# Kernel optimization log

Measured on AMD Instinct MI355X. Metric: run time of the kernel, lower is better.

Reference implementation:

```python
import jax, jax.numpy as jnp
import numpy as np


def setup_inputs() -> dict:
    key = jax.random.key(0)
    k1, k2, k3, k4 = jax.random.split(key, 4)
    N, C_in, C_out, H, W, K = 32, 128, 256, 56, 56, 3
    x = jax.random.normal(k1, (N, C_in, H, W), dtype=jnp.float32)
    # ternary weights in {-1, 0, +1}, stored as int8 like the torch buffer
    w_q = jax.random.randint(k2, (C_out, C_in, K, K), -1, 2).astype(jnp.int8)
    s = jax.random.uniform(k3, (C_out, 1, 1), dtype=jnp.float32) + 0.5
    bias = jax.random.normal(k4, (C_out,), dtype=jnp.float32)
    return {"x": x, "w_q": w_q, "s": s, "bias": bias}


def reference(x, w_q, s, bias):
    # y = conv2d(x, w_q.float()) * s + bias, stride=1, padding=1, dilation=1, groups=1
    w = w_q.astype(x.dtype)  # ternary {-1,0,+1} cast to float, as in torch
    y = jax.lax.conv_general_dilated(
        x, w,
        window_strides=(1, 1),
        padding=((1, 1), (1, 1)),
        lhs_dilation=(1, 1),
        rhs_dilation=(1, 1),
        dimension_numbers=("NCHW", "OIHW", "NCHW"),
        feature_group_count=1,
    )
    y = y * s  # s: [C_out,1,1] broadcasts over [N,C_out,H,W]
    y = y + bias.reshape(1, -1, 1, 1)
    return y
```

## Files before the change

### kernel.cpp

```cpp
#include <hip/hip_runtime.h>
#include <hip/hip_bf16.h>

typedef unsigned short ushort_t;

#define N_IMG 32
#define C_IN  128
#define C_OUT 256
#define H_SZ  56
#define W_SZ  56
#define HW_SZ (H_SZ * W_SZ)
#define K_TOT (C_IN * 9)
#define WP 64
#define HP 58
#define ROW_E (WP * C_IN)

typedef __attribute__((ext_vector_type(8))) short bf16x8;
typedef __attribute__((ext_vector_type(4))) float floatx4;

__device__ __forceinline__ void gl_lds16(const ushort_t* g, ushort_t* l) {
  __builtin_amdgcn_global_load_lds(
      (const __attribute__((address_space(1))) void*)g,
      (__attribute__((address_space(3))) void*)l, 16, 0, 0);
}

__device__ __forceinline__ ushort_t f2bf(float f) {
  __hip_bfloat16 b = __float2bfloat16(f);
  return *reinterpret_cast<ushort_t*>(&b);
}

__global__ void wtrans_kernel(const int* __restrict__ wq, ushort_t* __restrict__ wt) {
  int idx = blockIdx.x * 256 + threadIdx.x;
  if (idx >= C_OUT * K_TOT) return;
  int co = idx / K_TOT;
  int k  = idx - co * K_TOT;
  int tap = k >> 7;
  int c   = k & 127;
  int kh = tap / 3, kw = tap - kh * 3;
  int v = wq[((co * C_IN + c) * 3 + kh) * 3 + kw];
  wt[idx] = f2bf((float)v);
}

__global__ __launch_bounds__(256) void xpad_kernel(const float* __restrict__ x,
                                                   ushort_t* __restrict__ xp) {
  int b = blockIdx.x;
  int t = threadIdx.x;
  ushort_t* row = xp + (size_t)b * ROW_E;
  int n = b / HP;
  int h1 = b - n * HP;
  if (b >= N_IMG * HP || h1 == 0 || h1 == HP - 1) {
    uint4 z = {0u, 0u, 0u, 0u};
    uint4* r4 = (uint4*)row;
#pragma unroll
    for (int i = 0; i < 4; ++i) r4[i * 256 + t] = z;
    return;
  }
  __shared__ float tile[C_IN * 57];
  int h = h1 - 1;
  const float* xb = x + (size_t)n * C_IN * HW_SZ + h * W_SZ;
#pragma unroll
  for (int i = 0; i < 7; ++i) {
    int idx = i * 256 + t;
    int c = idx / 14, f = idx - c * 14;
    float4 v = *(const float4*)(xb + (size_t)c * HW_SZ + f * 4);
    float* dst = &tile[c * 57 + f * 4];
    dst[0] = v.x; dst[1] = v.y; dst[2] = v.z; dst[3] = v.w;
  }
  __syncthreads();
  unsigned int* r32 = (unsigned int*)row;
#pragma unroll
  for (int i = 0; i < 16; ++i) {
    int idx = i * 256 + t;
    int wp = idx >> 6, cp = idx & 63;
    unsigned int u = 0;
    if (wp >= 1 && wp <= W_SZ) {
      int w = wp - 1;
      u = (unsigned int)f2bf(tile[(2 * cp) * 57 + w]) |
          ((unsigned int)f2bf(tile[(2 * cp + 1) * 57 + w]) << 16);
    }
    r32[wp * 64 + cp] = u;
  }
}

__global__ __launch_bounds__(256) void bitconv_kernel(
    const ushort_t* __restrict__ wt, const ushort_t* __restrict__ xp,
    const float* __restrict__ s, const float* __restrict__ bias,
    float* __restrict__ out) {
  __shared__ ushort_t As[2][128 * 64];
  __shared__ ushort_t Bs[2][128 * 64];

  int d = blockIdx.x;
  int xcd = d & 7;
  int r   = d >> 3;
  int co0 = (r & 1) * 128;
  int sp_tile = xcd * 112 + (r >> 1);
  int nh0 = sp_tile * 2;
  int n  = nh0 / H_SZ;
  int hh = nh0 - n * H_SZ;

  int tid  = threadIdx.x;
  int lane = tid & 63;
  int wid  = tid >> 6;
  int l15  = lane & 15;
  int quad = lane >> 4;
  int wave_m = (wid >> 1) * 64;
  int wave_n = (wid & 1) * 64;

  int qoff = (((lane & 7) ^ (lane >> 3)) * 8);
  const ushort_t* a_src[4];
  const ushort_t* b_src[4];
  int dst_e[4];
#pragma unroll
  for (int g = 0; g < 4; ++g) {
    int rrow = wid * 32 + g * 8 + (lane >> 3);
    a_src[g] = wt + (size_t)(co0 + rrow) * K_TOT + qoff;
    int hrow = rrow >> 6, wpp = (rrow & 63) + 1;
    b_src[g] = xp + (size_t)((n * HP + hh + 1 + hrow) * WP + wpp) * C_IN + qoff;
    dst_e[g] = (wid * 32 + g * 8) * 64;
  }

  int koff0 = (quad ^ (l15 & 7)) * 8;
  int koff1 = koff0 ^ 32;

  floatx4 acc[4][4];
#pragma unroll
  for (int mi = 0; mi < 4; ++mi)
#pragma unroll
    for (int ni = 0; ni < 4; ++ni)
      acc[mi][ni] = (floatx4){0.f, 0.f, 0.f, 0.f};

  auto stage = [&](int tap, int half, int buf) {
    int aoff = tap * C_IN + half * 64;
    int boff = (tap / 3 - 1) * ROW_E + (tap % 3 - 1) * C_IN + half * 64;
#pragma unroll
    for (int g = 0; g < 4; ++g) {
      gl_lds16(a_src[g] + aoff, &As[buf][dst_e[g]]);
      gl_lds16(b_src[g] + boff, &Bs[buf][dst_e[g]]);
    }
  };

  stage(0, 0, 0);
#pragma unroll
  for (int st = 0; st < 18; ++st) {
    int buf = st & 1;
    if (st < 17) {
      stage((st + 1) >> 1, (st + 1) & 1, buf ^ 1);
      asm volatile("s_waitcnt vmcnt(8)" ::: "memory");
    } else {
      asm volatile("s_waitcnt vmcnt(0)" ::: "memory");
    }
    __builtin_amdgcn_s_barrier();
    asm volatile("" ::: "memory");

#pragma unroll
    for (int ks = 0; ks < 2; ++ks) {
      int ko = ks ? koff1 : koff0;
      bf16x8 af[4], bfv[4];
#pragma unroll
      for (int mi = 0; mi < 4; ++mi)
        af[mi] = *(const bf16x8*)&As[buf][(wave_m + mi * 16 + l15) * 64 + ko];
#pragma unroll
      for (int ni = 0; ni < 4; ++ni)
        bfv[ni] = *(const bf16x8*)&Bs[buf][(wave_n + ni * 16 + l15) * 64 + ko];
#pragma unroll
      for (int mi = 0; mi < 4; ++mi)
#pragma unroll
        for (int ni = 0; ni < 4; ++ni)
          acc[mi][ni] = __builtin_amdgcn_mfma_f32_16x16x32_bf16(
              af[mi], bfv[ni], acc[mi][ni], 0, 0, 0);
    }

    asm volatile("" ::: "memory");
    __builtin_amdgcn_s_barrier();
    asm volatile("" ::: "memory");
  }

  int h_out = hh + (wid & 1);
#pragma unroll
  for (int mi = 0; mi < 4; ++mi) {
#pragma unroll
    for (int rg = 0; rg < 4; ++rg) {
      int co = co0 + wave_m + mi * 16 + quad * 4 + rg;
      float sv = s[co];
      float bv = bias[co];
      float* ob = out + (size_t)(n * C_OUT + co) * HW_SZ + h_out * W_SZ;
#pragma unroll
      for (int ni = 0; ni < 4; ++ni) {
        int wpp = ni * 16 + l15;
        if (wpp < W_SZ)
          ob[wpp] = acc[mi][ni][rg] * sv + bv;
      }
    }
  }
}

extern "C" void kernel_launch(void* const* d_in, const int* in_sizes, int n_in,
                              void* d_out, int out_size, void* d_ws, size_t ws_size,
                              hipStream_t stream) {
  const float* x    = (const float*)d_in[0];
  const int*   wq   = (const int*)d_in[1];
  const float* s    = (const float*)d_in[2];
  const float* bias = (const float*)d_in[3];
  float* out = (float*)d_out;

  char* ws = (char*)d_ws;
  ushort_t* wt = (ushort_t*)ws;
  ushort_t* xp = (ushort_t*)(ws + 589824);

  hipLaunchKernelGGL(wtrans_kernel, dim3((C_OUT * K_TOT) / 256), dim3(256), 0, stream,
                     wq, wt);
  hipLaunchKernelGGL(xpad_kernel, dim3(N_IMG * HP + 1), dim3(256), 0, stream, x, xp);
  hipLaunchKernelGGL(bitconv_kernel, dim3(1792), dim3(256), 0, stream,
                     wt, xp, s, bias, out);
}
```

Measured before the change: 216.7 us.

## Enlarge conv GEMM tile to 256x256 with 8-wave ping-pong MFMA schedule

Moves the bitconv kernel from 128x128 tiles with 4 waves to 256x256 tiles (all output channels by four image rows) with 8 waves per 512-thread block. The main loop becomes a ping-pong schedule that interleaves LDS fragment loads, staged global-to-LDS copies, barriers and setprio-raised MFMA bursts across four quadrant sub-steps. The aim is more data reuse per loaded byte and better overlap of memory traffic with matrix math. In exchange it uses 128 KB of LDS, more accumulator registers and only 448 blocks, which may leave CUs underused.

```diff
diff --git a/kernel.cpp b/kernel.cpp
--- a/kernel.cpp
+++ b/kernel.cpp
@@ -81,113 +81,202 @@
   }
 }
 
-__global__ __launch_bounds__(256) void bitconv_kernel(
+__global__ __launch_bounds__(512, 2) void bitconv_kernel(
     const ushort_t* __restrict__ wt, const ushort_t* __restrict__ xp,
     const float* __restrict__ s, const float* __restrict__ bias,
     float* __restrict__ out) {
-  __shared__ ushort_t As[2][128 * 64];
-  __shared__ ushort_t Bs[2][128 * 64];
+  __shared__ ushort_t As[2 * 16384];
+  __shared__ ushort_t Bs[2 * 16384];
 
   int d = blockIdx.x;
-  int xcd = d & 7;
-  int r   = d >> 3;
-  int co0 = (r & 1) * 128;
-  int sp_tile = xcd * 112 + (r >> 1);
-  int nh0 = sp_tile * 2;
-  int n  = nh0 / H_SZ;
-  int hh = nh0 - n * H_SZ;
+  int sp_tile = (d & 7) * 56 + (d >> 3);
 
   int tid  = threadIdx.x;
   int lane = tid & 63;
   int wid  = tid >> 6;
   int l15  = lane & 15;
   int quad = lane >> 4;
-  int wave_m = (wid >> 1) * 64;
-  int wave_n = (wid & 1) * 64;
-
-  int qoff = (((lane & 7) ^ (lane >> 3)) * 8);
-  const ushort_t* a_src[4];
-  const ushort_t* b_src[4];
-  int dst_e[4];
-#pragma unroll
-  for (int g = 0; g < 4; ++g) {
-    int rrow = wid * 32 + g * 8 + (lane >> 3);
-    a_src[g] = wt + (size_t)(co0 + rrow) * K_TOT + qoff;
-    int hrow = rrow >> 6, wpp = (rrow & 63) + 1;
-    b_src[g] = xp + (size_t)((n * HP + hh + 1 + hrow) * WP + wpp) * C_IN + qoff;
-    dst_e[g] = (wid * 32 + g * 8) * 64;
-  }
-
-  int koff0 = (quad ^ (l15 & 7)) * 8;
-  int koff1 = koff0 ^ 32;
-
-  floatx4 acc[4][4];
-#pragma unroll
-  for (int mi = 0; mi < 4; ++mi)
+  int wave_m = (wid >> 2) * 128;
+  int wave_n = (wid & 3) * 64;
+
+  int qoff = ((lane & 7) ^ (lane >> 3)) * 8;
+  const ushort_t* a_base = wt + (size_t)(tid >> 3) * K_TOT + qoff;
+  const ushort_t* b_base[2][2];
+#pragma unroll
+  for (int h = 0; h < 2; ++h)
+#pragma unroll
+    for (int s2 = 0; s2 < 2; ++s2) {
+      int nh = sp_tile * 4 + h * 2 + s2;
+      int n  = nh / H_SZ, hi = nh - n * H_SZ;
+      b_base[h][s2] =
+          xp + (size_t)((n * HP + 1 + hi) * WP + (tid >> 3) + 1) * C_IN + qoff;
+    }
+  int sd00 = (0 * 128 + 0 * 64 + wid * 8) * 64;
+  int sd01 = (0 * 128 + 1 * 64 + wid * 8) * 64;
+  int sd10 = (1 * 128 + 0 * 64 + wid * 8) * 64;
+  int sd11 = (1 * 128 + 1 * 64 + wid * 8) * 64;
+
+  int ko0 = (quad ^ (l15 & 7)) * 8;
+  int ko1 = ko0 ^ 32;
+  int ar = (wave_m + l15) * 64;
+  int br = (wave_n + l15) * 64;
+
+  floatx4 acc[8][4];
+#pragma unroll
+  for (int mi = 0; mi < 8; ++mi)
 #pragma unroll
     for (int ni = 0; ni < 4; ++ni)
       acc[mi][ni] = (floatx4){0.f, 0.f, 0.f, 0.f};
 
-  auto stage = [&](int tap, int half, int buf) {
-    int aoff = tap * C_IN + half * 64;
-    int boff = (tap / 3 - 1) * ROW_E + (tap % 3 - 1) * C_IN + half * 64;
-#pragma unroll
-    for (int g = 0; g < 4; ++g) {
-      gl_lds16(a_src[g] + aoff, &As[buf][dst_e[g]]);
-      gl_lds16(b_src[g] + boff, &Bs[buf][dst_e[g]]);
-    }
+  auto stageA = [&](int NB, int s_aoff) {
+    gl_lds16(a_base + 0 * K_TOT + s_aoff,                 &As[NB + sd00]);
+    gl_lds16(a_base + 64 * K_TOT + s_aoff,                &As[NB + sd01]);
+    gl_lds16(a_base + 128 * K_TOT + s_aoff,               &As[NB + sd10]);
+    gl_lds16(a_base + 192 * K_TOT + s_aoff,               &As[NB + sd11]);
   };
-
-  stage(0, 0, 0);
-#pragma unroll
-  for (int st = 0; st < 18; ++st) {
-    int buf = st & 1;
-    if (st < 17) {
-      stage((st + 1) >> 1, (st + 1) & 1, buf ^ 1);
-      asm volatile("s_waitcnt vmcnt(8)" ::: "memory");
+  auto stageB = [&](int NB, int s_boff) {
+    gl_lds16(b_base[0][0] + s_boff, &Bs[NB + sd00]);
+    gl_lds16(b_base[0][1] + s_boff, &Bs[NB + sd01]);
+    gl_lds16(b_base[1][0] + s_boff, &Bs[NB + sd10]);
+    gl_lds16(b_base[1][1] + s_boff, &Bs[NB + sd11]);
+  };
+
+  auto tile = [&](int AB, int NB, int s_aoff, int s_boff, bool do_stage) {
+    bf16x8 af[4][2], bn0[2][2], bn1[2][2];
+    if (do_stage) {
+      stageA(NB, s_aoff);
+      asm volatile("s_waitcnt vmcnt(4)" ::: "memory");
     } else {
       asm volatile("s_waitcnt vmcnt(0)" ::: "memory");
     }
     __builtin_amdgcn_s_barrier();
     asm volatile("" ::: "memory");
-
-#pragma unroll
-    for (int ks = 0; ks < 2; ++ks) {
-      int ko = ks ? koff1 : koff0;
-      bf16x8 af[4], bfv[4];
-#pragma unroll
-      for (int mi = 0; mi < 4; ++mi)
-        af[mi] = *(const bf16x8*)&As[buf][(wave_m + mi * 16 + l15) * 64 + ko];
-#pragma unroll
-      for (int ni = 0; ni < 4; ++ni)
-        bfv[ni] = *(const bf16x8*)&Bs[buf][(wave_n + ni * 16 + l15) * 64 + ko];
-#pragma unroll
-      for (int mi = 0; mi < 4; ++mi)
-#pragma unroll
-        for (int ni = 0; ni < 4; ++ni)
+#pragma unroll
+    for (int mi = 0; mi < 4; ++mi) {
+      af[mi][0] = *(const bf16x8*)&As[AB + ar + mi * 1024 + ko0];
+      af[mi][1] = *(const bf16x8*)&As[AB + ar + mi * 1024 + ko1];
+    }
+#pragma unroll
+    for (int ni = 0; ni < 2; ++ni) {
+      bn0[ni][0] = *(const bf16x8*)&Bs[AB + br + ni * 1024 + ko0];
+      bn0[ni][1] = *(const bf16x8*)&Bs[AB + br + ni * 1024 + ko1];
+    }
+    asm volatile("s_waitcnt lgkmcnt(0)" ::: "memory");
+    __builtin_amdgcn_sched_barrier(0);
+    __builtin_amdgcn_s_setprio(1);
+#pragma unroll
+    for (int mi = 0; mi < 4; ++mi)
+#pragma unroll
+      for (int ni = 0; ni < 2; ++ni)
+#pragma unroll
+        for (int ks = 0; ks < 2; ++ks)
           acc[mi][ni] = __builtin_amdgcn_mfma_f32_16x16x32_bf16(
-              af[mi], bfv[ni], acc[mi][ni], 0, 0, 0);
-    }
-
-    asm volatile("" ::: "memory");
-    __builtin_amdgcn_s_barrier();
-    asm volatile("" ::: "memory");
-  }
-
-  int h_out = hh + (wid & 1);
-#pragma unroll
-  for (int mi = 0; mi < 4; ++mi) {
+              af[mi][ks], bn0[ni][ks], acc[mi][ni], 0, 0, 0);
+    __builtin_amdgcn_s_setprio(0);
+    asm volatile("" ::: "memory");
+    __builtin_amdgcn_s_barrier();
+    asm volatile("" ::: "memory");
+#pragma unroll
+    for (int ni = 0; ni < 2; ++ni) {
+      bn1[ni][0] = *(const bf16x8*)&Bs[AB + br + (2 + ni) * 1024 + ko0];
+      bn1[ni][1] = *(const bf16x8*)&Bs[AB + br + (2 + ni) * 1024 + ko1];
+    }
+    if (do_stage) stageB(NB, s_boff);
+    asm volatile("" ::: "memory");
+    __builtin_amdgcn_s_barrier();
+    asm volatile("s_waitcnt lgkmcnt(0)" ::: "memory");
+    __builtin_amdgcn_sched_barrier(0);
+    __builtin_amdgcn_s_setprio(1);
+#pragma unroll
+    for (int mi = 0; mi < 4; ++mi)
+#pragma unroll
+      for (int ni = 0; ni < 2; ++ni)
+#pragma unroll
+        for (int ks = 0; ks < 2; ++ks)
+          acc[mi][2 + ni] = __builtin_amdgcn_mfma_f32_16x16x32_bf16(
+              af[mi][ks], bn1[ni][ks], acc[mi][2 + ni], 0, 0, 0);
+    __builtin_amdgcn_s_setprio(0);
+    asm volatile("" ::: "memory");
+    __builtin_amdgcn_s_barrier();
+    asm volatile("" ::: "memory");
+#pragma unroll
+    for (int mi = 0; mi < 4; ++mi) {
+      af[mi][0] = *(const bf16x8*)&As[AB + ar + (4 + mi) * 1024 + ko0];
+      af[mi][1] = *(const bf16x8*)&As[AB + ar + (4 + mi) * 1024 + ko1];
+    }
+    asm volatile("" ::: "memory");
+    __builtin_amdgcn_s_barrier();
+    asm volatile("s_waitcnt lgkmcnt(0)" ::: "memory");
+    __builtin_amdgcn_sched_barrier(0);
+    __builtin_amdgcn_s_setprio(1);
+#pragma unroll
+    for (int mi = 0; mi < 4; ++mi)
+#pragma unroll
+      for (int ni = 0; ni < 2; ++ni)
+#pragma unroll
+        for (int ks = 0; ks < 2; ++ks)
+          acc[4 + mi][2 + ni] = __builtin_amdgcn_mfma_f32_16x16x32_bf16(
+              af[mi][ks], bn1[ni][ks], acc[4 + mi][2 + ni], 0, 0, 0);
+    __builtin_amdgcn_s_setprio(0);
+    asm volatile("" ::: "memory");
+    __builtin_amdgcn_s_barrier();
+    asm volatile("" ::: "memory");
+#pragma unroll
+    for (int ni = 0; ni < 2; ++ni) {
+      bn0[ni][0] = *(const bf16x8*)&Bs[AB + br + ni * 1024 + ko0];
+      bn0[ni][1] = *(const bf16x8*)&Bs[AB + br + ni * 1024 + ko1];
+    }
+    asm volatile("" ::: "memory");
+    __builtin_amdgcn_s_barrier();
+    asm volatile("s_waitcnt lgkmcnt(0)" ::: "memory");
+    __builtin_amdgcn_sched_barrier(0);
+    __builtin_amdgcn_s_setprio(1);
+#pragma unroll
+    for (int mi = 0; mi < 4; ++mi)
+#pragma unroll
+      for (int ni = 0; ni < 2; ++ni)
+#pragma unroll
+        for (int ks = 0; ks < 2; ++ks)
+          acc[4 + mi][ni] = __builtin_amdgcn_mfma_f32_16x16x32_bf16(
+              af[mi][ks], bn0[ni][ks], acc[4 + mi][ni], 0, 0, 0);
+    __builtin_amdgcn_s_setprio(0);
+    asm volatile("" ::: "memory");
+    __builtin_amdgcn_s_barrier();
+    asm volatile("" ::: "memory");
+  };
+
+  stageA(0, 0);
+  stageB(0, -ROW_E - C_IN);
+
+#pragma unroll 1
+  for (int kh = -1; kh <= 1; ++kh) {
+#pragma unroll 1
+    for (int kw = -1; kw <= 1; ++kw) {
+      int tapidx = (kh + 1) * 3 + (kw + 1);
+      bool last = (kh == 1) && (kw == 1);
+      int nkh = (kw == 1) ? kh + 1 : kh;
+      int nkw = (kw == 1) ? -1 : kw + 1;
+      tile(0, 16384, tapidx * 128 + 64, kh * ROW_E + kw * C_IN + 64, true);
+      tile(16384, 0, (tapidx + 1) * 128, nkh * ROW_E + nkw * C_IN, !last);
+    }
+  }
+
+  int nh_w = sp_tile * 4 + (wid & 3);
+  int n_out = nh_w / H_SZ, h_img = nh_w - n_out * H_SZ;
+  float* obase = out + (size_t)n_out * C_OUT * HW_SZ + h_img * W_SZ;
+#pragma unroll
+  for (int mi = 0; mi < 8; ++mi) {
 #pragma unroll
     for (int rg = 0; rg < 4; ++rg) {
-      int co = co0 + wave_m + mi * 16 + quad * 4 + rg;
+      int co = wave_m + mi * 16 + quad * 4 + rg;
       float sv = s[co];
       float bv = bias[co];
-      float* ob = out + (size_t)(n * C_OUT + co) * HW_SZ + h_out * W_SZ;
+      float* ob = obase + (size_t)co * HW_SZ;
 #pragma unroll
       for (int ni = 0; ni < 4; ++ni) {
-        int wpp = ni * 16 + l15;
-        if (wpp < W_SZ)
-          ob[wpp] = acc[mi][ni][rg] * sv + bv;
+        int w2 = ni * 16 + l15;
+        if (w2 < W_SZ)
+          ob[w2] = acc[mi][ni][rg] * sv + bv;
       }
     }
   }
@@ -209,6 +298,6 @@
   hipLaunchKernelGGL(wtrans_kernel, dim3((C_OUT * K_TOT) / 256), dim3(256), 0, stream,
                      wq, wt);
   hipLaunchKernelGGL(xpad_kernel, dim3(N_IMG * HP + 1), dim3(256), 0, stream, x, xp);
-  hipLaunchKernelGGL(bitconv_kernel, dim3(1792), dim3(256), 0, stream,
+  hipLaunchKernelGGL(bitconv_kernel, dim3(448), dim3(512), 0, stream,
                      wt, xp, s, bias, out);
 }
```

New measurement: 227.6 us. 5.0% more time.

## Enlarge conv GEMM tile to 256x256 with 512-thread blocks

Applied to the files above, without the earlier changes.

Each block now covers all 256 output channels and four spatial rows (256 pixels) using 8 waves, instead of a 128x128 tile with 4 waves. Each wave computes a 128x64 sub-tile with 8x4 accumulators, and the A fragment loads are split into two halves. The goal is to double operand reuse per LDS byte and cut redundant global loads of weights and activations. The cost is more registers per thread and more LDS (128KB double-buffered), and the grid shrinks to 448 blocks, which may underfill 256 CUs and limit occupancy.

```diff
diff --git a/kernel.cpp b/kernel.cpp
--- a/kernel.cpp
+++ b/kernel.cpp
@@ -81,69 +81,78 @@
   }
 }
 
-__global__ __launch_bounds__(256) void bitconv_kernel(
+__global__ __launch_bounds__(512, 2) void bitconv_kernel(
     const ushort_t* __restrict__ wt, const ushort_t* __restrict__ xp,
     const float* __restrict__ s, const float* __restrict__ bias,
     float* __restrict__ out) {
-  __shared__ ushort_t As[2][128 * 64];
-  __shared__ ushort_t Bs[2][128 * 64];
+  __shared__ ushort_t As[2 * 16384];
+  __shared__ ushort_t Bs[2 * 16384];
 
   int d = blockIdx.x;
-  int xcd = d & 7;
-  int r   = d >> 3;
-  int co0 = (r & 1) * 128;
-  int sp_tile = xcd * 112 + (r >> 1);
-  int nh0 = sp_tile * 2;
-  int n  = nh0 / H_SZ;
-  int hh = nh0 - n * H_SZ;
+  int sp_tile = (d & 7) * 56 + (d >> 3);
 
   int tid  = threadIdx.x;
   int lane = tid & 63;
   int wid  = tid >> 6;
   int l15  = lane & 15;
   int quad = lane >> 4;
-  int wave_m = (wid >> 1) * 64;
-  int wave_n = (wid & 1) * 64;
-
-  int qoff = (((lane & 7) ^ (lane >> 3)) * 8);
-  const ushort_t* a_src[4];
-  const ushort_t* b_src[4];
-  int dst_e[4];
-#pragma unroll
-  for (int g = 0; g < 4; ++g) {
-    int rrow = wid * 32 + g * 8 + (lane >> 3);
-    a_src[g] = wt + (size_t)(co0 + rrow) * K_TOT + qoff;
-    int hrow = rrow >> 6, wpp = (rrow & 63) + 1;
-    b_src[g] = xp + (size_t)((n * HP + hh + 1 + hrow) * WP + wpp) * C_IN + qoff;
-    dst_e[g] = (wid * 32 + g * 8) * 64;
-  }
-
-  int koff0 = (quad ^ (l15 & 7)) * 8;
-  int koff1 = koff0 ^ 32;
-
-  floatx4 acc[4][4];
-#pragma unroll
-  for (int mi = 0; mi < 4; ++mi)
+  int wave_m = (wid >> 2) * 128;
+  int wave_n = (wid & 3) * 64;
+
+  int qoff = ((lane & 7) ^ (lane >> 3)) * 8;
+  const ushort_t* a_base = wt + (size_t)(tid >> 3) * K_TOT + qoff;
+  const ushort_t* b_base[2][2];
+#pragma unroll
+  for (int h = 0; h < 2; ++h)
+#pragma unroll
+    for (int s2 = 0; s2 < 2; ++s2) {
+      int nh = sp_tile * 4 + h * 2 + s2;
+      int n  = nh / H_SZ, hi = nh - n * H_SZ;
+      b_base[h][s2] =
+          xp + (size_t)((n * HP + 1 + hi) * WP + (tid >> 3) + 1) * C_IN + qoff;
+    }
+  int sd0 = (0 * 64 + wid * 8) * 64;
+  int sd1 = (1 * 64 + wid * 8) * 64;
+  int sd2 = (2 * 64 + wid * 8) * 64;
+  int sd3 = (3 * 64 + wid * 8) * 64;
+
+  int ko0 = (quad ^ (l15 & 7)) * 8;
+  int ko1 = ko0 ^ 32;
+  int ar = (wave_m + l15) * 64;
+  int br = (wave_n + l15) * 64;
+
+  floatx4 acc[8][4];
+#pragma unroll
+  for (int mi = 0; mi < 8; ++mi)
 #pragma unroll
     for (int ni = 0; ni < 4; ++ni)
       acc[mi][ni] = (floatx4){0.f, 0.f, 0.f, 0.f};
 
-  auto stage = [&](int tap, int half, int buf) {
-    int aoff = tap * C_IN + half * 64;
-    int boff = (tap / 3 - 1) * ROW_E + (tap % 3 - 1) * C_IN + half * 64;
-#pragma unroll
-    for (int g = 0; g < 4; ++g) {
-      gl_lds16(a_src[g] + aoff, &As[buf][dst_e[g]]);
-      gl_lds16(b_src[g] + boff, &Bs[buf][dst_e[g]]);
-    }
+  auto stageA = [&](int NB, int s_aoff) {
+    gl_lds16(a_base + 0 * K_TOT + s_aoff,   &As[NB + sd0]);
+    gl_lds16(a_base + 64 * K_TOT + s_aoff,  &As[NB + sd1]);
+    gl_lds16(a_base + 128 * K_TOT + s_aoff, &As[NB + sd2]);
+    gl_lds16(a_base + 192 * K_TOT + s_aoff, &As[NB + sd3]);
   };
-
-  stage(0, 0, 0);
-#pragma unroll
-  for (int st = 0; st < 18; ++st) {
-    int buf = st & 1;
-    if (st < 17) {
-      stage((st + 1) >> 1, (st + 1) & 1, buf ^ 1);
+  auto stageB = [&](int NB, int s_boff) {
+    gl_lds16(b_base[0][0] + s_boff, &Bs[NB + sd0]);
+    gl_lds16(b_base[0][1] + s_boff, &Bs[NB + sd1]);
+    gl_lds16(b_base[1][0] + s_boff, &Bs[NB + sd2]);
+    gl_lds16(b_base[1][1] + s_boff, &Bs[NB + sd3]);
+  };
+
+  stageA(0, 0);
+  stageB(0, -ROW_E - C_IN);
+
+#pragma unroll
+  for (int kt = 0; kt < 18; ++kt) {
+    int cb = (kt & 1) * 16384;
+    int nb = 16384 - cb;
+    if (kt < 17) {
+      int ntap  = (kt + 1) >> 1;
+      int nhalf = (kt + 1) & 1;
+      stageA(nb, ntap * C_IN + nhalf * 64);
+      stageB(nb, (ntap / 3 - 1) * ROW_E + (ntap % 3 - 1) * C_IN + nhalf * 64);
       asm volatile("s_waitcnt vmcnt(8)" ::: "memory");
     } else {
       asm volatile("s_waitcnt vmcnt(0)" ::: "memory");
@@ -151,43 +160,60 @@
     __builtin_amdgcn_s_barrier();
     asm volatile("" ::: "memory");
 
-#pragma unroll
-    for (int ks = 0; ks < 2; ++ks) {
-      int ko = ks ? koff1 : koff0;
-      bf16x8 af[4], bfv[4];
-#pragma unroll
-      for (int mi = 0; mi < 4; ++mi)
-        af[mi] = *(const bf16x8*)&As[buf][(wave_m + mi * 16 + l15) * 64 + ko];
+    bf16x8 bfv[4][2], af[4][2];
+#pragma unroll
+    for (int ni = 0; ni < 4; ++ni) {
+      bfv[ni][0] = *(const bf16x8*)&Bs[cb + br + ni * 1024 + ko0];
+      bfv[ni][1] = *(const bf16x8*)&Bs[cb + br + ni * 1024 + ko1];
+    }
+#pragma unroll
+    for (int mi = 0; mi < 4; ++mi) {
+      af[mi][0] = *(const bf16x8*)&As[cb + ar + mi * 1024 + ko0];
+      af[mi][1] = *(const bf16x8*)&As[cb + ar + mi * 1024 + ko1];
+    }
+#pragma unroll
+    for (int mi = 0; mi < 4; ++mi)
 #pragma unroll
       for (int ni = 0; ni < 4; ++ni)
-        bfv[ni] = *(const bf16x8*)&Bs[buf][(wave_n + ni * 16 + l15) * 64 + ko];
-#pragma unroll
-      for (int mi = 0; mi < 4; ++mi)
-#pragma unroll
-        for (int ni = 0; ni < 4; ++ni)
+#pragma unroll
+        for (int ks = 0; ks < 2; ++ks)
           acc[mi][ni] = __builtin_amdgcn_mfma_f32_16x16x32_bf16(
-              af[mi], bfv[ni], acc[mi][ni], 0, 0, 0);
-    }
+              af[mi][ks], bfv[ni][ks], acc[mi][ni], 0, 0, 0);
+#pragma unroll
+    for (int mi = 0; mi < 4; ++mi) {
+      af[mi][0] = *(const bf16x8*)&As[cb + ar + (4 + mi) * 1024 + ko0];
+      af[mi][1] = *(const bf16x8*)&As[cb + ar + (4 + mi) * 1024 + ko1];
+    }
+#pragma unroll
+    for (int mi = 0; mi < 4; ++mi)
+#pragma unroll
+      for (int ni = 0; ni < 4; ++ni)
+#pragma unroll
+        for (int ks = 0; ks < 2; ++ks)
+          acc[4 + mi][ni] = __builtin_amdgcn_mfma_f32_16x16x32_bf16(
+              af[mi][ks], bfv[ni][ks], acc[4 + mi][ni], 0, 0, 0);
 
     asm volatile("" ::: "memory");
     __builtin_amdgcn_s_barrier();
     asm volatile("" ::: "memory");
   }
 
-  int h_out = hh + (wid & 1);
-#pragma unroll
-  for (int mi = 0; mi < 4; ++mi) {
+  int nh_w = sp_tile * 4 + (wid & 3);
+  int n_out = nh_w / H_SZ, h_img = nh_w - n_out * H_SZ;
+  float* obase = out + (size_t)n_out * C_OUT * HW_SZ + h_img * W_SZ;
+#pragma unroll
+  for (int mi = 0; mi < 8; ++mi) {
 #pragma unroll
     for (int rg = 0; rg < 4; ++rg) {
-      int co = co0 + wave_m + mi * 16 + quad * 4 + rg;
+      int co = wave_m + mi * 16 + quad * 4 + rg;
       float sv = s[co];
       float bv = bias[co];
-      float* ob = out + (size_t)(n * C_OUT + co) * HW_SZ + h_out * W_SZ;
+      float* ob = obase + (size_t)co * HW_SZ;
 #pragma unroll
       for (int ni = 0; ni < 4; ++ni) {
-        int wpp = ni * 16 + l15;
-        if (wpp < W_SZ)
-          ob[wpp] = acc[mi][ni][rg] * sv + bv;
+        int w2 = ni * 16 + l15;
+        if (w2 < W_SZ)
+          ob[w2] = acc[mi][ni][rg] * sv + bv;
       }
     }
   }
@@ -209,6 +235,6 @@
   hipLaunchKernelGGL(wtrans_kernel, dim3((C_OUT * K_TOT) / 256), dim3(256), 0, stream,
                      wq, wt);
   hipLaunchKernelGGL(xpad_kernel, dim3(N_IMG * HP + 1), dim3(256), 0, stream, x, xp);
-  hipLaunchKernelGGL(bitconv_kernel, dim3(1792), dim3(256), 0, stream,
+  hipLaunchKernelGGL(bitconv_kernel, dim3(448), dim3(512), 0, stream,
                      wt, xp, s, bias, out);
 }
```

Result: no change. 215.4 us (-0.6%).
